# Kernel optimization log

Hardware: AMD Instinct MI355X
Metric: run time of the kernel (lower is better)

The kernel has to match this reference:

```python
import jax, jax.numpy as jnp
import numpy as np

V, E, C, H = 50000, 300, 128, 128
B, SC, SE = 128, 512, 64


def gru_scan(x, lengths, gate_w, gate_b, cand_w, cand_b):
    """TF GRUCell dynamic_rnn: x [B,S,E] -> outputs [B,S,C], zeroed past lengths."""
    Bn, S, _ = x.shape
    Cn = cand_w.shape[1]

    def step(h, inp):
        xt, t = inp  # xt [B,E]
        ru = jax.nn.sigmoid(jnp.concatenate([xt, h], axis=-1) @ gate_w + gate_b)
        r, u = jnp.split(ru, 2, axis=-1)
        c = jnp.tanh(jnp.concatenate([xt, r * h], axis=-1) @ cand_w + cand_b)
        hn = u * h + (1.0 - u) * c
        active = (t < lengths)[:, None]
        hn = jnp.where(active, hn, h)
        out = jnp.where(active, hn, 0.0)
        return hn, out

    h0 = jnp.zeros((Bn, Cn), dtype=x.dtype)
    _, outs = jax.lax.scan(step, h0, (jnp.swapaxes(x, 0, 1), jnp.arange(S)))
    return jnp.swapaxes(outs, 0, 1)


def reverse_seq(x, lengths):
    """tf.reverse_sequence along time for [B,S,D]."""
    S = x.shape[1]
    t = jnp.arange(S)[None, :]
    L = lengths[:, None]
    idx = jnp.where(t < L, L - 1 - t, t)
    return jnp.take_along_axis(x, idx[:, :, None], axis=1)


def attend(states, att_v, att_w, att_b):
    # states [B,S,C]
    scores = jnp.einsum('bsd,d->bs', jnp.tanh(jnp.einsum('bsc,cd->bsd', states, att_w) + att_b), att_v)
    w = jax.nn.softmax(scores, axis=1)
    return jnp.einsum('bsc,bs->bc', states, w)


def extract_features(seq, lengths, embeddings,
                     fw_gate_w, fw_gate_b, fw_cand_w, fw_cand_b,
                     bw_gate_w, bw_gate_b, bw_cand_w, bw_cand_b,
                     att_v, att_w, att_b):
    emb = embeddings[seq]  # [B,S,E]
    fw_states = gru_scan(emb, lengths, fw_gate_w, fw_gate_b, fw_cand_w, fw_cand_b)
    emb_rev = reverse_seq(emb, lengths)
    bw_out = gru_scan(emb_rev, lengths, bw_gate_w, bw_gate_b, bw_cand_w, bw_cand_b)
    bw_states = reverse_seq(bw_out, lengths)
    fw_c = attend(fw_states, att_v, att_w, att_b)
    bw_c = attend(bw_states, att_v, att_w, att_b)
    return jnp.concatenate([fw_c, bw_c], axis=1)


def setup_inputs() -> dict:
    key = jax.random.key(0)
    ks = jax.random.split(key, 20)
    s = 0.05
    context = jax.random.randint(ks[0], (B, SC), 0, V, dtype=jnp.int32)
    end = jax.random.randint(ks[1], (B, SE), 0, V, dtype=jnp.int32)
    context_length = jnp.clip(jax.random.randint(ks[2], (B,), 1, SC + 1), 1, SC).astype(jnp.int32)
    end_length = jnp.clip(jax.random.randint(ks[3], (B,), 1, SE + 1), 1, SE).astype(jnp.int32)
    return {
        'context': context, 'end': end,
        'context_length': context_length, 'end_length': end_length,
        'embeddings': jax.random.normal(ks[4], (V, E), jnp.float32) * s,
        'fw_gate_w': jax.random.normal(ks[5], (E + C, 2 * C), jnp.float32) * s,
        'fw_gate_b': jnp.ones((2 * C,), jnp.float32),
        'fw_cand_w': jax.random.normal(ks[6], (E + C, C), jnp.float32) * s,
        'fw_cand_b': jnp.zeros((C,), jnp.float32),
        'bw_gate_w': jax.random.normal(ks[7], (E + C, 2 * C), jnp.float32) * s,
        'bw_gate_b': jnp.ones((2 * C,), jnp.float32),
        'bw_cand_w': jax.random.normal(ks[8], (E + C, C), jnp.float32) * s,
        'bw_cand_b': jnp.zeros((C,), jnp.float32),
        'att_v': jax.random.normal(ks[9], (C,), jnp.float32) * s,
        'att_w': jax.random.normal(ks[10], (C, C), jnp.float32) * s,
        'att_b': jnp.zeros((C,), jnp.float32),
        'hid_w': jax.random.normal(ks[11], (4 * C, H), jnp.float32) * s,
        'hid_b': jnp.zeros((H,), jnp.float32),
        'out_w': jax.random.normal(ks[12], (H, 1), jnp.float32) * s,
        'out_b': jnp.zeros((1,), jnp.float32),
    }


def reference(context, end, context_length, end_length, embeddings,
              fw_gate_w, fw_gate_b, fw_cand_w, fw_cand_b,
              bw_gate_w, bw_gate_b, bw_cand_w, bw_cand_b,
              att_v, att_w, att_b, hid_w, hid_b, out_w, out_b):
    ctx_f = extract_features(context, context_length, embeddings,
                             fw_gate_w, fw_gate_b, fw_cand_w, fw_cand_b,
                             bw_gate_w, bw_gate_b, bw_cand_w, bw_cand_b,
                             att_v, att_w, att_b)
    end_f = extract_features(end, end_length, embeddings,
                             fw_gate_w, fw_gate_b, fw_cand_w, fw_cand_b,
                             bw_gate_w, bw_gate_b, bw_cand_w, bw_cand_b,
                             att_v, att_w, att_b)
    feats = jnp.concatenate([ctx_f, end_f], axis=1)  # [B, 4C]
    hidden = jax.nn.relu(feats @ hid_w + hid_b)
    logit = (hidden @ out_w + out_b)[:, 0]  # [B]
    return logit
```

## Files before the change

### kernel.cpp

```cpp
#include <hip/hip_runtime.h>
#include <cstdint>
#include <cmath>

static constexpr int V_  = 50000;
static constexpr int E_  = 300;
static constexpr int C_  = 128;
static constexpr int B_  = 128;
static constexpr int SC_ = 512;
static constexpr int SE_ = 64;
static constexpr int NCOL = 768;
static constexpr int KP  = 320;

static constexpr size_t OFF_PROJ  = 0;
static constexpr size_t SZ_PROJ   = (size_t)V_ * NCOL;
static constexpr size_t OFF_WXP   = OFF_PROJ + SZ_PROJ;
static constexpr size_t SZ_WXP    = (size_t)304 * NCOL;
static constexpr size_t OFF_UALL  = OFF_WXP + SZ_WXP;
static constexpr size_t SZ_UALL   = (size_t)C_ * NCOL;
static constexpr size_t OFF_BIAS  = OFF_UALL + SZ_UALL;
static constexpr size_t SZ_BIAS   = NCOL;
static constexpr size_t OFF_ST    = OFF_BIAS + SZ_BIAS;
static constexpr size_t SZ_ST_CTX = (size_t)B_ * SC_ * C_;
static constexpr size_t SZ_ST_END = (size_t)B_ * SE_ * C_;
static constexpr size_t SZ_ST     = 2*SZ_ST_CTX + 2*SZ_ST_END;
static constexpr size_t OFF_FEATS = OFF_ST + SZ_ST;
static constexpr size_t SZ_FEATS  = (size_t)B_ * 512;
static constexpr size_t OFF_BT    = OFF_FEATS + SZ_FEATS;
static constexpr size_t SZ_BT     = (size_t)NCOL * KP / 2 * 2;
static constexpr size_t OFF_AWT   = OFF_BT + SZ_BT;

typedef __attribute__((ext_vector_type(8))) short bf16x8;
typedef __attribute__((ext_vector_type(4))) float f32x4;

static __device__ __forceinline__ unsigned short f2bf_rne(float f) {
  unsigned u = __float_as_uint(f);
  unsigned r = u + 0x7fffu + ((u >> 16) & 1u);
  return (unsigned short)(r >> 16);
}

static __device__ __forceinline__ void gload_lds16(const short* g, short* l) {
  __builtin_amdgcn_global_load_lds(
      (const __attribute__((address_space(1))) void*)g,
      (__attribute__((address_space(3))) void*)l, 16, 0, 0);
}

static __device__ __forceinline__ float fast_sigmoid(float x) {
  return __builtin_amdgcn_rcpf(1.f + __expf(-x));
}
static __device__ __forceinline__ float fast_tanh(float x) {
  return fmaf(-2.f, __builtin_amdgcn_rcpf(__expf(2.f * x) + 1.f), 1.f);
}

__global__ void pack_kernel(const float* __restrict__ fw_gw, const float* __restrict__ fw_gb,
                            const float* __restrict__ fw_cw, const float* __restrict__ fw_cb,
                            const float* __restrict__ bw_gw, const float* __restrict__ bw_gb,
                            const float* __restrict__ bw_cw, const float* __restrict__ bw_cb,
                            float* __restrict__ ws) {
  int i = blockIdx.x * 256 + threadIdx.x;
  float* Wxp  = ws + OFF_WXP;
  float* Uall = ws + OFF_UALL;
  float* bias = ws + OFF_BIAS;
  if (i < 304 * NCOL) {
    int k = i / NCOL, c = i % NCOL;
    float v = 0.f;
    if (k < 300) {
      if (c < 256)      v = fw_gw[k*256 + c];
      else if (c < 384) v = fw_cw[k*128 + (c-256)];
      else if (c < 640) v = bw_gw[k*256 + (c-384)];
      else              v = bw_cw[k*128 + (c-640)];
    }
    Wxp[i] = v;
    return;
  }
  int j = i - 304 * NCOL;
  if (j >= 0 && j < 128 * NCOL) {
    int k = j / NCOL, c = j % NCOL;
    int kk = 300 + k;
    float v;
    if (c < 256)      v = fw_gw[kk*256 + c];
    else if (c < 384) v = fw_cw[kk*128 + (c-256)];
    else if (c < 640) v = bw_gw[kk*256 + (c-384)];
    else              v = bw_cw[kk*128 + (c-640)];
    Uall[j] = v;
    return;
  }
  int m = j - 128 * NCOL;
  if (m >= 0 && m < NCOL) {
    float v;
    if (m < 256)      v = fw_gb[m];
    else if (m < 384) v = fw_cb[m-256];
    else if (m < 640) v = bw_gb[m-384];
    else              v = bw_cb[m-640];
    bias[m] = v;
  }
}

__global__ void pack_bt(const float* __restrict__ Wxp, short* __restrict__ Bthi,
                        short* __restrict__ Btlo, const float* __restrict__ att_w,
                        short* __restrict__ awt_hi, short* __restrict__ awt_lo) {
  int i = blockIdx.x * 256 + threadIdx.x;
  if (i < NCOL * KP) {
    int k = i % KP, n = i / KP;
    float v = (k < 304) ? Wxp[(size_t)k * NCOL + n] : 0.f;
    unsigned short h = f2bf_rne(v);
    float hf = __uint_as_float((unsigned)h << 16);
    unsigned short lo = f2bf_rne(v - hf);
    Bthi[i] = (short)h;
    Btlo[i] = (short)lo;
    return;
  }
  int j = i - NCOL * KP;
  if (j < 128 * 128) {
    int d = j >> 7, c = j & 127;
    float v = att_w[(size_t)c * 128 + d];
    unsigned short h = f2bf_rne(v);
    float hf = __uint_as_float((unsigned)h << 16);
    unsigned short lo = f2bf_rne(v - hf);
    awt_hi[j] = (short)h;
    awt_lo[j] = (short)lo;
  }
}

__global__ void pack_emb(const float* __restrict__ emb, short* __restrict__ Ahi,
                         short* __restrict__ Alo) {
  size_t i = (size_t)blockIdx.x * 256 + threadIdx.x;
  if (i >= (size_t)V_ * KP) return;
  int k = (int)(i % KP);
  size_t row = i / KP;
  float v = (k < E_) ? emb[row * E_ + k] : 0.f;
  unsigned short h = f2bf_rne(v);
  float hf = __uint_as_float((unsigned)h << 16);
  unsigned short lo = f2bf_rne(v - hf);
  Ahi[i] = (short)h;
  Alo[i] = (short)lo;
}

__global__ __launch_bounds__(256) void gemm_mfma(
    const short* __restrict__ Ahi, const short* __restrict__ Alo,
    const short* __restrict__ Bthi, const short* __restrict__ Btlo,
    float* __restrict__ proj) {
  __shared__ short lds[16384];
  int tid = threadIdx.x, wid = tid >> 6, lane = tid & 63;
  int n0 = blockIdx.x * 128, m0 = blockIdx.y * 128;
  f32x4 acc[4][4] = {};

  int lr = lane >> 2, lc = lane & 3;
  int q0 = wid * 2, q1 = q0 + 1;
  int r0 = q0 * 16 + lr, r1 = q1 * 16 + lr;
  int am0 = m0 + r0; if (am0 > V_ - 1) am0 = V_ - 1;
  int am1 = m0 + r1; if (am1 > V_ - 1) am1 = V_ - 1;
  size_t gaOff0 = (size_t)am0 * KP + lc * 8;
  size_t gaOff1 = (size_t)am1 * KP + lc * 8;
  size_t gbOff0 = (size_t)(n0 + r0) * KP + lc * 8;
  size_t gbOff1 = (size_t)(n0 + r1) * KP + lc * 8;

  int quad = lane >> 4;
  int arow = (wid >> 1) * 64 + (lane & 15);
  int brow = (wid & 1) * 64 + (lane & 15);

  for (int k0 = 0; k0 < KP; k0 += 32) {
    gload_lds16(Ahi  + gaOff0 + k0, lds +         q0 * 512);
    gload_lds16(Ahi  + gaOff1 + k0, lds +         q1 * 512);
    gload_lds16(Alo  + gaOff0 + k0, lds +  4096 + q0 * 512);
    gload_lds16(Alo  + gaOff1 + k0, lds +  4096 + q1 * 512);
    gload_lds16(Bthi + gbOff0 + k0, lds +  8192 + q0 * 512);
    gload_lds16(Bthi + gbOff1 + k0, lds +  8192 + q1 * 512);
    gload_lds16(Btlo + gbOff0 + k0, lds + 12288 + q0 * 512);
    gload_lds16(Btlo + gbOff1 + k0, lds + 12288 + q1 * 512);
    __syncthreads();

    bf16x8 ah[4], al[4], bh[4], bl[4];
#pragma unroll
    for (int i = 0; i < 4; ++i) {
      ah[i] = *(bf16x8*)&lds[        (arow + i*16) * 32 + quad * 8];
      al[i] = *(bf16x8*)&lds[ 4096 + (arow + i*16) * 32 + quad * 8];
      bh[i] = *(bf16x8*)&lds[ 8192 + (brow + i*16) * 32 + quad * 8];
      bl[i] = *(bf16x8*)&lds[12288 + (brow + i*16) * 32 + quad * 8];
    }
#pragma unroll
    for (int i = 0; i < 4; ++i)
#pragma unroll
      for (int j = 0; j < 4; ++j) {
        acc[i][j] = __builtin_amdgcn_mfma_f32_16x16x32_bf16(ah[i], bh[j], acc[i][j], 0, 0, 0);
        acc[i][j] = __builtin_amdgcn_mfma_f32_16x16x32_bf16(ah[i], bl[j], acc[i][j], 0, 0, 0);
        acc[i][j] = __builtin_amdgcn_mfma_f32_16x16x32_bf16(al[i], bh[j], acc[i][j], 0, 0, 0);
      }
    __syncthreads();
  }

  int colb = n0 + (wid & 1) * 64 + (lane & 15);
  int rowb = m0 + (wid >> 1) * 64 + quad * 4;
#pragma unroll
  for (int i = 0; i < 4; ++i) {
    int rb = rowb + i * 16;
#pragma unroll
    for (int j = 0; j < 4; ++j) {
      int cc = colb + j * 16;
#pragma unroll
      for (int r = 0; r < 4; ++r) {
        int rr = rb + r;
        if (rr < V_) proj[(size_t)rr * NCOL + cc] = acc[i][j][r];
      }
    }
  }
}

__global__ __attribute__((amdgpu_flat_work_group_size(256, 256),
                          amdgpu_waves_per_eu(2, 2)))
void recur_kernel(
    const int* __restrict__ ctx, const int* __restrict__ endseq,
    const int* __restrict__ ctx_len, const int* __restrict__ end_len,
    const float* __restrict__ proj, const float* __restrict__ Uall,
    const float* __restrict__ bias, float* __restrict__ states) {
  __shared__ __align__(16) float h_s[128];
  __shared__ __align__(16) float rh_s[128];
  __shared__ __align__(16) float u_s[128];
  __shared__ __align__(16) float pg[8][260];
  __shared__ __align__(16) float pc[8][132];

  int bid = blockIdx.x;
  int tid = threadIdx.x;
  const int* seq; int S, L, b, dir; float* stbase;
  if (bid < 256) {
    b = bid >> 1; dir = bid & 1;
    seq = ctx + b * SC_; S = SC_; L = ctx_len[b];
    stbase = states + (dir ? SZ_ST_CTX : 0) + (size_t)b * SC_ * C_;
  } else {
    int q = bid - 256; b = q >> 1; dir = q & 1;
    seq = endseq + b * SE_; S = SE_; L = end_len[b];
    stbase = states + 2*SZ_ST_CTX + (dir ? SZ_ST_END : 0) + (size_t)b * SE_ * C_;
  }
  int dirOff = dir ? 384 : 0;
  int kg = tid >> 5, jg = tid & 31;

  float wg[16][8];
  float wc[16][4];
#pragma unroll
  for (int kk = 0; kk < 16; ++kk) {
    const float* up = Uall + (size_t)(kg*16 + kk) * NCOL + dirOff;
    float4 w0 = *(const float4*)(up + jg*8);
    float4 w1 = *(const float4*)(up + jg*8 + 4);
    wg[kk][0]=w0.x; wg[kk][1]=w0.y; wg[kk][2]=w0.z; wg[kk][3]=w0.w;
    wg[kk][4]=w1.x; wg[kk][5]=w1.y; wg[kk][6]=w1.z; wg[kk][7]=w1.w;
    float4 wv = *(const float4*)(up + 256 + jg*4);
    wc[kk][0]=wv.x; wc[kk][1]=wv.y; wc[kk][2]=wv.z; wc[kk][3]=wv.w;
  }
  float bias_g = bias[dirOff + tid];
  float bias_c = (tid < 128) ? bias[dirOff + 256 + tid] : 0.f;

  if (tid < 128) h_s[tid] = 0.f;
  __syncthreads();

  int pos0 = dir ? (L - 1) : 0;
  int tok0 = seq[pos0];
  const float* xr0 = proj + (size_t)tok0 * NCOL + dirOff;
  float xg = xr0[tid];
  float xc = (tid < 128) ? xr0[256 + tid] : 0.f;

  for (int t = 0; t < L; ++t) {
    float xg_n = 0.f, xc_n = 0.f;
    if (t + 1 < L) {
      int pos_n = dir ? (L - 2 - t) : (t + 1);
      int tok_n = seq[pos_n];
      const float* xr = proj + (size_t)tok_n * NCOL + dirOff;
      xg_n = xr[tid];
      xc_n = (tid < 128) ? xr[256 + tid] : 0.f;
    }

    float a[8] = {0.f,0.f,0.f,0.f,0.f,0.f,0.f,0.f};
    const float4* h4 = (const float4*)h_s;
#pragma unroll
    for (int q = 0; q < 4; ++q) {
      float4 hv = h4[kg*4 + q];
      float he[4] = {hv.x, hv.y, hv.z, hv.w};
#pragma unroll
      for (int e = 0; e < 4; ++e)
#pragma unroll
        for (int jj = 0; jj < 8; ++jj)
          a[jj] += he[e] * wg[q*4 + e][jj];
    }
    *(float4*)(&pg[kg][jg*8])     = make_float4(a[0], a[1], a[2], a[3]);
    *(float4*)(&pg[kg][jg*8 + 4]) = make_float4(a[4], a[5], a[6], a[7]);
    __syncthreads();

    float g = xg + bias_g;
#pragma unroll
    for (int k2 = 0; k2 < 8; ++k2) g += pg[k2][tid];
    g = fast_sigmoid(g);

    float h_old = 0.f;
    if (tid < 128) { h_old = h_s[tid]; rh_s[tid] = g * h_old; }
    else           { u_s[tid - 128] = g; }
    __syncthreads();

    float ac[4] = {0.f, 0.f, 0.f, 0.f};
    const float4* rh4 = (const float4*)rh_s;
#pragma unroll
    for (int q = 0; q < 4; ++q) {
      float4 rv = rh4[kg*4 + q];
      float re[4] = {rv.x, rv.y, rv.z, rv.w};
#pragma unroll
      for (int e = 0; e < 4; ++e)
#pragma unroll
        for (int jj = 0; jj < 4; ++jj)
          ac[jj] += re[e] * wc[q*4 + e][jj];
    }
    *(float4*)(&pc[kg][jg*4]) = make_float4(ac[0], ac[1], ac[2], ac[3]);
    __syncthreads();

    if (tid < 128) {
      float cs = xc + bias_c;
#pragma unroll
      for (int k2 = 0; k2 < 8; ++k2) cs += pc[k2][tid];
      float c = fast_tanh(cs);
      float u = u_s[tid];
      float hn = u * h_old + (1.f - u) * c;
      h_s[tid] = hn;
      int pos = dir ? (L - 1 - t) : t;
      stbase[(size_t)pos * C_ + tid] = hn;
    }
    __syncthreads();
    xg = xg_n; xc = xc_n;
  }

  for (int i = L * C_ + tid; i < S * C_; i += 256) stbase[i] = 0.f;
}

__global__ __launch_bounds__(256, 2) void attn_kernel(
    const float* __restrict__ states, const short* __restrict__ awt_hi,
    const short* __restrict__ awt_lo, const float* __restrict__ att_v,
    const float* __restrict__ att_b, float* __restrict__ feats) {
  __shared__ __align__(16) float st_s[16][132];
  __shared__ __align__(16) short ah_s[16][132];
  __shared__ __align__(16) short al_s[16][132];
  __shared__ float spart[4][16];
  __shared__ float score_s[16];
  __shared__ float cm[128], cl[128], ca[128];

  int bid = blockIdx.x, tid = threadIdx.x;
  int b, dir, S, featOff; const float* stb;
  if (bid < 256) {
    b = bid >> 1; dir = bid & 1; S = SC_;
    stb = states + (dir ? SZ_ST_CTX : 0) + (size_t)b * SC_ * C_;
    featOff = dir * 128;
  } else {
    int q = bid - 256; b = q >> 1; dir = q & 1; S = SE_;
    stb = states + 2*SZ_ST_CTX + (dir ? SZ_ST_END : 0) + (size_t)b * SE_ * C_;
    featOff = 256 + dir * 128;
  }

  int w = tid >> 6, lane = tid & 63;
  int quad = lane >> 4, l15 = lane & 15;

  int d0 = 32 * w + l15, d1 = d0 + 16;
  bf16x8 bh0[4], bh1[4], bl0[4], bl1[4];
#pragma unroll
  for (int kt = 0; kt < 4; ++kt) {
    bh0[kt] = *(const bf16x8*)&awt_hi[d0*128 + kt*32 + quad*8];
    bh1[kt] = *(const bf16x8*)&awt_hi[d1*128 + kt*32 + quad*8];
    bl0[kt] = *(const bf16x8*)&awt_lo[d0*128 + kt*32 + quad*8];
    bl1[kt] = *(const bf16x8*)&awt_lo[d1*128 + kt*32 + quad*8];
  }
  float vv0 = att_v[d0], vv1 = att_v[d1];
  float bb0 = att_b[d0], bb1 = att_b[d1];

  int c = tid & 127, half = tid >> 7;
  float m = -1e30f, lsum = 0.f, acc = 0.f;

  int lrow = tid >> 4, lcol = (tid & 15) * 8;
  float4 p0, p1;
  {
    const float* src = stb + (size_t)lrow * C_ + lcol;
    p0 = *(const float4*)(src);
    p1 = *(const float4*)(src + 4);
  }

  int nchunks = S >> 4;
  for (int ch = 0; ch < nchunks; ++ch) {
    __syncthreads();
    float f[8] = {p0.x, p0.y, p0.z, p0.w, p1.x, p1.y, p1.z, p1.w};
    short hi8[8], lo8[8];
#pragma unroll
    for (int j = 0; j < 8; ++j) {
      unsigned short h = f2bf_rne(f[j]);
      float hf = __uint_as_float((unsigned)h << 16);
      hi8[j] = (short)h;
      lo8[j] = (short)f2bf_rne(f[j] - hf);
    }
    *(float4*)(&st_s[lrow][lcol])     = p0;
    *(float4*)(&st_s[lrow][lcol + 4]) = p1;
    *(bf16x8*)(&ah_s[lrow][lcol]) = *(bf16x8*)hi8;
    *(bf16x8*)(&al_s[lrow][lcol]) = *(bf16x8*)lo8;
    if (ch + 1 < nchunks) {
      const float* src = stb + (size_t)((ch + 1) * 16 + lrow) * C_ + lcol;
      p0 = *(const float4*)(src);
      p1 = *(const float4*)(src + 4);
    }
    __syncthreads();

    f32x4 ac0 = {0.f, 0.f, 0.f, 0.f}, ac1 = {0.f, 0.f, 0.f, 0.f};
#pragma unroll
    for (int kt = 0; kt < 4; ++kt) {
      bf16x8 a_hi = *(bf16x8*)&ah_s[l15][kt*32 + quad*8];
      bf16x8 a_lo = *(bf16x8*)&al_s[l15][kt*32 + quad*8];
      ac0 = __builtin_amdgcn_mfma_f32_16x16x32_bf16(a_hi, bh0[kt], ac0, 0, 0, 0);
      ac0 = __builtin_amdgcn_mfma_f32_16x16x32_bf16(a_hi, bl0[kt], ac0, 0, 0, 0);
      ac0 = __builtin_amdgcn_mfma_f32_16x16x32_bf16(a_lo, bh0[kt], ac0, 0, 0, 0);
      ac1 = __builtin_amdgcn_mfma_f32_16x16x32_bf16(a_hi, bh1[kt], ac1, 0, 0, 0);
      ac1 = __builtin_amdgcn_mfma_f32_16x16x32_bf16(a_hi, bl1[kt], ac1, 0, 0, 0);
      ac1 = __builtin_amdgcn_mfma_f32_16x16x32_bf16(a_lo, bh1[kt], ac1, 0, 0, 0);
    }

    float part[4];
#pragma unroll
    for (int r = 0; r < 4; ++r)
      part[r] = fast_tanh(ac0[r] + bb0) * vv0 + fast_tanh(ac1[r] + bb1) * vv1;
#pragma unroll
    for (int mask = 1; mask <= 8; mask <<= 1)
#pragma unroll
      for (int r = 0; r < 4; ++r)
        part[r] += __shfl_xor(part[r], mask, 64);
    if (l15 == 0) {
#pragma unroll
      for (int r = 0; r < 4; ++r) spart[w][quad*4 + r] = part[r];
    }
    __syncthreads();
    if (tid < 16)
      score_s[tid] = spart[0][tid] + spart[1][tid] + spart[2][tid] + spart[3][tid];
    __syncthreads();

    float srow[8]; float smax = m;
#pragma unroll
    for (int r = 0; r < 8; ++r) { srow[r] = score_s[half*8 + r]; smax = fmaxf(smax, srow[r]); }
    float scale = __expf(m - smax);
    acc *= scale; lsum *= scale; m = smax;
#pragma unroll
    for (int r = 0; r < 8; ++r) {
      float wgt = __expf(srow[r] - m);
      lsum += wgt;
      acc += wgt * st_s[half*8 + r][c];
    }
  }

  __syncthreads();
  if (half == 1) { cm[c] = m; cl[c] = lsum; ca[c] = acc; }
  __syncthreads();
  if (half == 0) {
    float m1 = cm[c], l1 = cl[c], a1 = ca[c];
    float M = fmaxf(m, m1);
    float w0 = __expf(m - M), w1 = __expf(m1 - M);
    feats[b * 512 + featOff + c] = (acc * w0 + a1 * w1) / (lsum * w0 + l1 * w1);
  }
}

__global__ __launch_bounds__(128) void head_kernel(
    const float* __restrict__ feats, const float* __restrict__ hid_w,
    const float* __restrict__ hid_b, const float* __restrict__ out_w,
    const float* __restrict__ out_b, float* __restrict__ out) {
  __shared__ __align__(16) float f_s[512];
  __shared__ float part[2];
  int b = blockIdx.x, tid = threadIdx.x;
  for (int i = tid; i < 512; i += 128) f_s[i] = feats[b * 512 + i];
  __syncthreads();
  float h = hid_b[tid];
  for (int k = 0; k < 512; ++k) h += f_s[k] * hid_w[k * 128 + tid];
  h = fmaxf(h, 0.f);
  float p = h * out_w[tid];
#pragma unroll
  for (int off = 32; off > 0; off >>= 1) p += __shfl_xor(p, off, 64);
  if ((tid & 63) == 0) part[tid >> 6] = p;
  __syncthreads();
  if (tid == 0) out[b] = part[0] + part[1] + out_b[0];
}

extern "C" void kernel_launch(void* const* d_in, const int* in_sizes, int n_in,
                              void* d_out, int out_size, void* d_ws, size_t ws_size,
                              hipStream_t stream) {
  const int*   ctx     = (const int*)d_in[0];
  const int*   endseq  = (const int*)d_in[1];
  const int*   ctx_len = (const int*)d_in[2];
  const int*   end_len = (const int*)d_in[3];
  const float* emb     = (const float*)d_in[4];
  const float* fw_gw   = (const float*)d_in[5];
  const float* fw_gb   = (const float*)d_in[6];
  const float* fw_cw   = (const float*)d_in[7];
  const float* fw_cb   = (const float*)d_in[8];
  const float* bw_gw   = (const float*)d_in[9];
  const float* bw_gb   = (const float*)d_in[10];
  const float* bw_cw   = (const float*)d_in[11];
  const float* bw_cb   = (const float*)d_in[12];
  const float* att_v   = (const float*)d_in[13];
  const float* att_w   = (const float*)d_in[14];
  const float* att_b   = (const float*)d_in[15];
  const float* hid_w   = (const float*)d_in[16];
  const float* hid_b   = (const float*)d_in[17];
  const float* out_w   = (const float*)d_in[18];
  const float* out_b   = (const float*)d_in[19];
  float* ws  = (float*)d_ws;
  float* out = (float*)d_out;

  short* Ahi    = (short*)(ws + OFF_ST);
  short* Alo    = Ahi + (size_t)V_ * KP;
  short* Bthi   = (short*)(ws + OFF_BT);
  short* Btlo   = Bthi + (size_t)NCOL * KP;
  short* awt_hi = (short*)(ws + OFF_AWT);
  short* awt_lo = awt_hi + 128 * 128;

  pack_kernel<<<1299, 256, 0, stream>>>(fw_gw, fw_gb, fw_cw, fw_cb,
                                        bw_gw, bw_gb, bw_cw, bw_cb, ws);
  pack_bt<<<(NCOL * KP + 128 * 128 + 255) / 256, 256, 0, stream>>>(
      ws + OFF_WXP, Bthi, Btlo, att_w, awt_hi, awt_lo);
  pack_emb<<<(int)(((size_t)V_ * KP + 255) / 256), 256, 0, stream>>>(emb, Ahi, Alo);

  dim3 ggrid(6, 391);
  gemm_mfma<<<ggrid, 256, 0, stream>>>(Ahi, Alo, Bthi, Btlo, ws + OFF_PROJ);

  recur_kernel<<<512, 256, 0, stream>>>(ctx, endseq, ctx_len, end_len,
                                        ws + OFF_PROJ, ws + OFF_UALL,
                                        ws + OFF_BIAS, ws + OFF_ST);

  attn_kernel<<<512, 256, 0, stream>>>(ws + OFF_ST, awt_hi, awt_lo,
                                       att_v, att_b, ws + OFF_FEATS);

  head_kernel<<<128, 128, 0, stream>>>(ws + OFF_FEATS, hid_w, hid_b,
                                       out_w, out_b, out);
}
```

Before: 768.4 us.

## Batch GRU recurrence over 16 sequences per block using split-bf16 MFMA

The recurrence kernel no longer runs one sequence per block with scalar FP32 dot products. It now handles 16 sequences per block (32 blocks in total) and computes the gate and candidate matmuls with bf16 MFMA, using a hi/lo split so the result stays close to FP32. This cuts the per-step synchronisations from four to two and replaces the VALU accumulation with matrix cores. The cost is that each block runs until the longest of its 16 sequences ends, and only 32 CUs are occupied. Separately, the projection GEMM switches to a 1D grid with an XCD-aware block remap to improve cache locality.

```diff
diff --git a/kernel.cpp b/kernel.cpp
--- a/kernel.cpp
+++ b/kernel.cpp
@@ -141,7 +141,13 @@
     float* __restrict__ proj) {
   __shared__ short lds[16384];
   int tid = threadIdx.x, wid = tid >> 6, lane = tid & 63;
-  int n0 = blockIdx.x * 128, m0 = blockIdx.y * 128;
+
+  int bid = blockIdx.x;
+  int xcd = bid & 7, idx = bid >> 3;
+  int wgid = (xcd < 2 ? xcd * 294 : 588 + (xcd - 2) * 293) + idx;
+  int m0 = (wgid / 6) * 128;
+  int n0 = (wgid % 6) * 128;
+
   f32x4 acc[4][4] = {};
 
   int lr = lane >> 2, lc = lane & 3;
@@ -206,124 +212,220 @@
 }
 
 __global__ __attribute__((amdgpu_flat_work_group_size(256, 256),
-                          amdgpu_waves_per_eu(2, 2)))
-void recur_kernel(
+                          amdgpu_waves_per_eu(1, 1)))
+void recur_mfma_kernel(
     const int* __restrict__ ctx, const int* __restrict__ endseq,
     const int* __restrict__ ctx_len, const int* __restrict__ end_len,
     const float* __restrict__ proj, const float* __restrict__ Uall,
     const float* __restrict__ bias, float* __restrict__ states) {
-  __shared__ __align__(16) float h_s[128];
-  __shared__ __align__(16) float rh_s[128];
-  __shared__ __align__(16) float u_s[128];
-  __shared__ __align__(16) float pg[8][260];
-  __shared__ __align__(16) float pc[8][132];
-
-  int bid = blockIdx.x;
-  int tid = threadIdx.x;
-  const int* seq; int S, L, b, dir; float* stbase;
-  if (bid < 256) {
-    b = bid >> 1; dir = bid & 1;
-    seq = ctx + b * SC_; S = SC_; L = ctx_len[b];
-    stbase = states + (dir ? SZ_ST_CTX : 0) + (size_t)b * SC_ * C_;
-  } else {
-    int q = bid - 256; b = q >> 1; dir = q & 1;
-    seq = endseq + b * SE_; S = SE_; L = end_len[b];
-    stbase = states + 2*SZ_ST_CTX + (dir ? SZ_ST_END : 0) + (size_t)b * SE_ * C_;
-  }
+  __shared__ __align__(16) short hAh[4][16][32];
+  __shared__ __align__(16) short hAl[4][16][32];
+  __shared__ __align__(16) short rAh[4][16][32];
+  __shared__ __align__(16) short rAl[4][16][32];
+  __shared__ __align__(16) float h_f[16][132];
+  __shared__ __align__(16) float u_f[16][132];
+
+  int g = blockIdx.x, tid = threadIdx.x;
+  int w = tid >> 6, lane = tid & 63, quad = lane >> 4, l15 = lane & 15;
+
+  int isEnd = (g >> 4) & 1, dir = (g >> 3) & 1;
+  int b0 = (g & 7) * 16;
+  int S = isEnd ? SE_ : SC_;
+  const int* seqarr = isEnd ? endseq : ctx;
+  const int* lenarr = isEnd ? end_len : ctx_len;
+  float* stroot = states + (isEnd ? (2*SZ_ST_CTX + (dir ? SZ_ST_END : 0))
+                                  : (dir ? SZ_ST_CTX : 0));
   int dirOff = dir ? 384 : 0;
-  int kg = tid >> 5, jg = tid & 31;
-
-  float wg[16][8];
-  float wc[16][4];
-#pragma unroll
-  for (int kk = 0; kk < 16; ++kk) {
-    const float* up = Uall + (size_t)(kg*16 + kk) * NCOL + dirOff;
-    float4 w0 = *(const float4*)(up + jg*8);
-    float4 w1 = *(const float4*)(up + jg*8 + 4);
-    wg[kk][0]=w0.x; wg[kk][1]=w0.y; wg[kk][2]=w0.z; wg[kk][3]=w0.w;
-    wg[kk][4]=w1.x; wg[kk][5]=w1.y; wg[kk][6]=w1.z; wg[kk][7]=w1.w;
-    float4 wv = *(const float4*)(up + 256 + jg*4);
-    wc[kk][0]=wv.x; wc[kk][1]=wv.y; wc[kk][2]=wv.z; wc[kk][3]=wv.w;
-  }
-  float bias_g = bias[dirOff + tid];
-  float bias_c = (tid < 128) ? bias[dirOff + 256 + tid] : 0.f;
-
-  if (tid < 128) h_s[tid] = 0.f;
+
+  const int* seqp[4]; int Lr[4]; float* stb[4];
+#pragma unroll
+  for (int r = 0; r < 4; ++r) {
+    int b = b0 + quad*4 + r;
+    seqp[r] = seqarr + b * S;
+    Lr[r]   = lenarr[b];
+    stb[r]  = stroot + (size_t)b * S * C_;
+  }
+  int Lm = Lr[0];
+#pragma unroll
+  for (int r = 1; r < 4; ++r) Lm = (Lr[r] > Lm) ? Lr[r] : Lm;
+  { int o = __shfl_xor(Lm, 16, 64); Lm = (o > Lm) ? o : Lm; }
+  { int o = __shfl_xor(Lm, 32, 64); Lm = (o > Lm) ? o : Lm; }
+
+  int colg[4], colc[2];
+#pragma unroll
+  for (int tt = 0; tt < 4; ++tt) colg[tt] = w*64 + tt*16 + l15;
+#pragma unroll
+  for (int tt = 0; tt < 2; ++tt) colc[tt] = w*32 + tt*16 + l15;
+
+  bf16x8 gBh[4][4], gBl[4][4], cBh[2][4], cBl[2][4];
+#pragma unroll
+  for (int tt = 0; tt < 4; ++tt)
+#pragma unroll
+    for (int kt = 0; kt < 4; ++kt) {
+      short h8[8], l8[8];
+#pragma unroll
+      for (int j = 0; j < 8; ++j) {
+        float v = Uall[(size_t)(kt*32 + quad*8 + j) * NCOL + dirOff + colg[tt]];
+        unsigned short hh = f2bf_rne(v);
+        float hf = __uint_as_float((unsigned)hh << 16);
+        h8[j] = (short)hh;
+        l8[j] = (short)f2bf_rne(v - hf);
+      }
+      gBh[tt][kt] = *(bf16x8*)h8;
+      gBl[tt][kt] = *(bf16x8*)l8;
+    }
+#pragma unroll
+  for (int tt = 0; tt < 2; ++tt)
+#pragma unroll
+    for (int kt = 0; kt < 4; ++kt) {
+      short h8[8], l8[8];
+#pragma unroll
+      for (int j = 0; j < 8; ++j) {
+        float v = Uall[(size_t)(kt*32 + quad*8 + j) * NCOL + dirOff + 256 + colc[tt]];
+        unsigned short hh = f2bf_rne(v);
+        float hf = __uint_as_float((unsigned)hh << 16);
+        h8[j] = (short)hh;
+        l8[j] = (short)f2bf_rne(v - hf);
+      }
+      cBh[tt][kt] = *(bf16x8*)h8;
+      cBl[tt][kt] = *(bf16x8*)l8;
+    }
+
+  float bg[4], bc[2];
+#pragma unroll
+  for (int tt = 0; tt < 4; ++tt) bg[tt] = bias[dirOff + colg[tt]];
+#pragma unroll
+  for (int tt = 0; tt < 2; ++tt) bc[tt] = bias[dirOff + 256 + colc[tt]];
+
+  for (int i = tid; i < 16*132; i += 256) ((float*)h_f)[i] = 0.f;
+  for (int i = tid; i < 4*16*32; i += 256) {
+    ((short*)hAh)[i] = 0; ((short*)hAl)[i] = 0;
+  }
   __syncthreads();
 
-  int pos0 = dir ? (L - 1) : 0;
-  int tok0 = seq[pos0];
-  const float* xr0 = proj + (size_t)tok0 * NCOL + dirOff;
-  float xg = xr0[tid];
-  float xc = (tid < 128) ? xr0[256 + tid] : 0.f;
-
-  for (int t = 0; t < L; ++t) {
-    float xg_n = 0.f, xc_n = 0.f;
-    if (t + 1 < L) {
-      int pos_n = dir ? (L - 2 - t) : (t + 1);
-      int tok_n = seq[pos_n];
-      const float* xr = proj + (size_t)tok_n * NCOL + dirOff;
-      xg_n = xr[tid];
-      xc_n = (tid < 128) ? xr[256 + tid] : 0.f;
-    }
-
-    float a[8] = {0.f,0.f,0.f,0.f,0.f,0.f,0.f,0.f};
-    const float4* h4 = (const float4*)h_s;
-#pragma unroll
-    for (int q = 0; q < 4; ++q) {
-      float4 hv = h4[kg*4 + q];
-      float he[4] = {hv.x, hv.y, hv.z, hv.w};
-#pragma unroll
-      for (int e = 0; e < 4; ++e)
-#pragma unroll
-        for (int jj = 0; jj < 8; ++jj)
-          a[jj] += he[e] * wg[q*4 + e][jj];
-    }
-    *(float4*)(&pg[kg][jg*8])     = make_float4(a[0], a[1], a[2], a[3]);
-    *(float4*)(&pg[kg][jg*8 + 4]) = make_float4(a[4], a[5], a[6], a[7]);
-    __syncthreads();
-
-    float g = xg + bias_g;
-#pragma unroll
-    for (int k2 = 0; k2 < 8; ++k2) g += pg[k2][tid];
-    g = fast_sigmoid(g);
-
-    float h_old = 0.f;
-    if (tid < 128) { h_old = h_s[tid]; rh_s[tid] = g * h_old; }
-    else           { u_s[tid - 128] = g; }
-    __syncthreads();
-
-    float ac[4] = {0.f, 0.f, 0.f, 0.f};
-    const float4* rh4 = (const float4*)rh_s;
-#pragma unroll
-    for (int q = 0; q < 4; ++q) {
-      float4 rv = rh4[kg*4 + q];
-      float re[4] = {rv.x, rv.y, rv.z, rv.w};
-#pragma unroll
-      for (int e = 0; e < 4; ++e)
-#pragma unroll
-        for (int jj = 0; jj < 4; ++jj)
-          ac[jj] += re[e] * wc[q*4 + e][jj];
-    }
-    *(float4*)(&pc[kg][jg*4]) = make_float4(ac[0], ac[1], ac[2], ac[3]);
-    __syncthreads();
-
-    if (tid < 128) {
-      float cs = xc + bias_c;
-#pragma unroll
-      for (int k2 = 0; k2 < 8; ++k2) cs += pc[k2][tid];
-      float c = fast_tanh(cs);
-      float u = u_s[tid];
-      float hn = u * h_old + (1.f - u) * c;
-      h_s[tid] = hn;
-      int pos = dir ? (L - 1 - t) : t;
-      stbase[(size_t)pos * C_ + tid] = hn;
-    }
-    __syncthreads();
-    xg = xg_n; xc = xc_n;
-  }
-
-  for (int i = L * C_ + tid; i < S * C_; i += 256) stbase[i] = 0.f;
+  auto load_x = [&](int stp, float (&XG)[4][4], float (&XC)[2][4]) {
+#pragma unroll
+    for (int r = 0; r < 4; ++r) {
+      int L = Lr[r];
+      int pos = (stp < L) ? (dir ? (L - 1 - stp) : stp) : 0;
+      int tok = seqp[r][pos];
+      const float* xr = proj + (size_t)tok * NCOL + dirOff;
+#pragma unroll
+      for (int tt = 0; tt < 4; ++tt) XG[tt][r] = xr[colg[tt]];
+#pragma unroll
+      for (int tt = 0; tt < 2; ++tt) XC[tt][r] = xr[256 + colc[tt]];
+    }
+  };
+
+  float xg[4][4], xc[2][4], xgn[4][4], xcn[2][4];
+  load_x(0, xg, xc);
+
+  for (int t = 0; t < Lm; ++t) {
+    load_x(t + 1, xgn, xcn);
+
+    f32x4 ag[4] = {};
+#pragma unroll
+    for (int kt = 0; kt < 4; ++kt) {
+      bf16x8 Ah = *(bf16x8*)&hAh[kt][l15][quad*8];
+      bf16x8 Al = *(bf16x8*)&hAl[kt][l15][quad*8];
+#pragma unroll
+      for (int tt = 0; tt < 4; ++tt)
+        ag[tt] = __builtin_amdgcn_mfma_f32_16x16x32_bf16(Ah, gBh[tt][kt], ag[tt], 0, 0, 0);
+#pragma unroll
+      for (int tt = 0; tt < 4; ++tt)
+        ag[tt] = __builtin_amdgcn_mfma_f32_16x16x32_bf16(Ah, gBl[tt][kt], ag[tt], 0, 0, 0);
+#pragma unroll
+      for (int tt = 0; tt < 4; ++tt)
+        ag[tt] = __builtin_amdgcn_mfma_f32_16x16x32_bf16(Al, gBh[tt][kt], ag[tt], 0, 0, 0);
+    }
+
+    if (w < 2) {
+#pragma unroll
+      for (int tt = 0; tt < 4; ++tt) {
+        int col = colg[tt];
+        int kt2 = col >> 5, kk = col & 31;
+#pragma unroll
+        for (int r = 0; r < 4; ++r) {
+          int row = quad*4 + r;
+          float gg = fast_sigmoid(ag[tt][r] + xg[tt][r] + bg[tt]);
+          float rh = gg * h_f[row][col];
+          unsigned short hi = f2bf_rne(rh);
+          float hf = __uint_as_float((unsigned)hi << 16);
+          rAh[kt2][row][kk] = (short)hi;
+          rAl[kt2][row][kk] = (short)f2bf_rne(rh - hf);
+        }
+      }
+    } else {
+#pragma unroll
+      for (int tt = 0; tt < 4; ++tt) {
+        int col = colg[tt] - 128;
+#pragma unroll
+        for (int r = 0; r < 4; ++r) {
+          int row = quad*4 + r;
+          float gg = fast_sigmoid(ag[tt][r] + xg[tt][r] + bg[tt]);
+          u_f[row][col] = gg;
+        }
+      }
+    }
+    __syncthreads();
+
+    f32x4 ac[2] = {};
+#pragma unroll
+    for (int kt = 0; kt < 4; ++kt) {
+      bf16x8 Ah = *(bf16x8*)&rAh[kt][l15][quad*8];
+      bf16x8 Al = *(bf16x8*)&rAl[kt][l15][quad*8];
+#pragma unroll
+      for (int tt = 0; tt < 2; ++tt)
+        ac[tt] = __builtin_amdgcn_mfma_f32_16x16x32_bf16(Ah, cBh[tt][kt], ac[tt], 0, 0, 0);
+#pragma unroll
+      for (int tt = 0; tt < 2; ++tt)
+        ac[tt] = __builtin_amdgcn_mfma_f32_16x16x32_bf16(Ah, cBl[tt][kt], ac[tt], 0, 0, 0);
+#pragma unroll
+      for (int tt = 0; tt < 2; ++tt)
+        ac[tt] = __builtin_amdgcn_mfma_f32_16x16x32_bf16(Al, cBh[tt][kt], ac[tt], 0, 0, 0);
+    }
+
+#pragma unroll
+    for (int tt = 0; tt < 2; ++tt) {
+      int col = colc[tt];
+      int kt2 = col >> 5, kk = col & 31;
+#pragma unroll
+      for (int r = 0; r < 4; ++r) {
+        int row = quad*4 + r;
+        float cs = ac[tt][r] + xc[tt][r] + bc[tt];
+        float cd = fast_tanh(cs);
+        float uu = u_f[row][col];
+        float ho = h_f[row][col];
+        float hn = uu * ho + (1.f - uu) * cd;
+        if (t < Lr[r]) {
+          h_f[row][col] = hn;
+          unsigned short hi = f2bf_rne(hn);
+          float hf = __uint_as_float((unsigned)hi << 16);
+          hAh[kt2][row][kk] = (short)hi;
+          hAl[kt2][row][kk] = (short)f2bf_rne(hn - hf);
+          int pos = dir ? (Lr[r] - 1 - t) : t;
+          stb[r][(size_t)pos * C_ + col] = hn;
+        }
+      }
+    }
+    __syncthreads();
+
+#pragma unroll
+    for (int tt = 0; tt < 4; ++tt)
+#pragma unroll
+      for (int r = 0; r < 4; ++r) xg[tt][r] = xgn[tt][r];
+#pragma unroll
+    for (int tt = 0; tt < 2; ++tt)
+#pragma unroll
+      for (int r = 0; r < 4; ++r) xc[tt][r] = xcn[tt][r];
+  }
+
+  for (int i = 0; i < 16; ++i) {
+    int b = b0 + i;
+    int L = lenarr[b];
+    float* sb = stroot + (size_t)b * S * C_;
+    for (int idx = L * C_ + tid; idx < S * C_; idx += 256) sb[idx] = 0.f;
+  }
 }
 
 __global__ __launch_bounds__(256, 2) void attn_kernel(
@@ -512,12 +614,11 @@
       ws + OFF_WXP, Bthi, Btlo, att_w, awt_hi, awt_lo);
   pack_emb<<<(int)(((size_t)V_ * KP + 255) / 256), 256, 0, stream>>>(emb, Ahi, Alo);
 
-  dim3 ggrid(6, 391);
-  gemm_mfma<<<ggrid, 256, 0, stream>>>(Ahi, Alo, Bthi, Btlo, ws + OFF_PROJ);
-
-  recur_kernel<<<512, 256, 0, stream>>>(ctx, endseq, ctx_len, end_len,
-                                        ws + OFF_PROJ, ws + OFF_UALL,
-                                        ws + OFF_BIAS, ws + OFF_ST);
+  gemm_mfma<<<2346, 256, 0, stream>>>(Ahi, Alo, Bthi, Btlo, ws + OFF_PROJ);
+
+  recur_mfma_kernel<<<32, 256, 0, stream>>>(ctx, endseq, ctx_len, end_len,
+                                            ws + OFF_PROJ, ws + OFF_UALL,
+                                            ws + OFF_BIAS, ws + OFF_ST);
 
   attn_kernel<<<512, 256, 0, stream>>>(ws + OFF_ST, awt_hi, awt_lo,
                                        att_v, att_b, ws + OFF_FEATS);
```

Measured after the change: 2.082 ms. 2.71x slower.

## Double recurrence block to 512 threads and remap GEMM tiles per XCD

Applied to the files above, without the earlier changes.

The GRU recurrence kernel now runs 512 threads per block. Each thread holds half as many recurrent-weight rows in registers, so the per-step serial matvec is shorter, and the 16 partial sums are combined with a tree reduction in LDS. Separately, the GEMM grid is flattened to 1D and block ids are remapped so each XCD gets a contiguous range of M-tiles, which should improve L2 reuse of the A rows shared across N-tiles. The cost is more threads per barrier and a longer reduction per step, and 512-thread blocks may lower residency in the recurrence.

```diff
diff --git a/kernel.cpp b/kernel.cpp
--- a/kernel.cpp
+++ b/kernel.cpp
@@ -141,7 +141,13 @@
     float* __restrict__ proj) {
   __shared__ short lds[16384];
   int tid = threadIdx.x, wid = tid >> 6, lane = tid & 63;
-  int n0 = blockIdx.x * 128, m0 = blockIdx.y * 128;
+
+  int bid = blockIdx.x;
+  int xcd = bid & 7, idx = bid >> 3;
+  int wgid = (xcd < 2 ? xcd * 294 : 588 + (xcd - 2) * 293) + idx;
+  int m0 = (wgid / 6) * 128;
+  int n0 = (wgid % 6) * 128;
+
   f32x4 acc[4][4] = {};
 
   int lr = lane >> 2, lc = lane & 3;
@@ -205,7 +211,7 @@
   }
 }
 
-__global__ __attribute__((amdgpu_flat_work_group_size(256, 256),
+__global__ __attribute__((amdgpu_flat_work_group_size(512, 512),
                           amdgpu_waves_per_eu(2, 2)))
 void recur_kernel(
     const int* __restrict__ ctx, const int* __restrict__ endseq,
@@ -215,8 +221,8 @@
   __shared__ __align__(16) float h_s[128];
   __shared__ __align__(16) float rh_s[128];
   __shared__ __align__(16) float u_s[128];
-  __shared__ __align__(16) float pg[8][260];
-  __shared__ __align__(16) float pc[8][132];
+  __shared__ __align__(16) float pg[16][260];
+  __shared__ __align__(16) float pc[16][132];
 
   int bid = blockIdx.x;
   int tid = threadIdx.x;
@@ -233,11 +239,11 @@
   int dirOff = dir ? 384 : 0;
   int kg = tid >> 5, jg = tid & 31;
 
-  float wg[16][8];
-  float wc[16][4];
-#pragma unroll
-  for (int kk = 0; kk < 16; ++kk) {
-    const float* up = Uall + (size_t)(kg*16 + kk) * NCOL + dirOff;
+  float wg[8][8];
+  float wc[8][4];
+#pragma unroll
+  for (int kk = 0; kk < 8; ++kk) {
+    const float* up = Uall + (size_t)(kg*8 + kk) * NCOL + dirOff;
     float4 w0 = *(const float4*)(up + jg*8);
     float4 w1 = *(const float4*)(up + jg*8 + 4);
     wg[kk][0]=w0.x; wg[kk][1]=w0.y; wg[kk][2]=w0.z; wg[kk][3]=w0.w;
@@ -245,7 +251,7 @@
     float4 wv = *(const float4*)(up + 256 + jg*4);
     wc[kk][0]=wv.x; wc[kk][1]=wv.y; wc[kk][2]=wv.z; wc[kk][3]=wv.w;
   }
-  float bias_g = bias[dirOff + tid];
+  float bias_g = (tid < 256) ? bias[dirOff + tid] : 0.f;
   float bias_c = (tid < 128) ? bias[dirOff + 256 + tid] : 0.f;
 
   if (tid < 128) h_s[tid] = 0.f;
@@ -254,7 +260,7 @@
   int pos0 = dir ? (L - 1) : 0;
   int tok0 = seq[pos0];
   const float* xr0 = proj + (size_t)tok0 * NCOL + dirOff;
-  float xg = xr0[tid];
+  float xg = (tid < 256) ? xr0[tid] : 0.f;
   float xc = (tid < 128) ? xr0[256 + tid] : 0.f;
 
   for (int t = 0; t < L; ++t) {
@@ -263,15 +269,15 @@
       int pos_n = dir ? (L - 2 - t) : (t + 1);
       int tok_n = seq[pos_n];
       const float* xr = proj + (size_t)tok_n * NCOL + dirOff;
-      xg_n = xr[tid];
-      xc_n = (tid < 128) ? xr[256 + tid] : 0.f;
+      if (tid < 256) xg_n = xr[tid];
+      if (tid < 128) xc_n = xr[256 + tid];
     }
 
     float a[8] = {0.f,0.f,0.f,0.f,0.f,0.f,0.f,0.f};
     const float4* h4 = (const float4*)h_s;
 #pragma unroll
-    for (int q = 0; q < 4; ++q) {
-      float4 hv = h4[kg*4 + q];
+    for (int q = 0; q < 2; ++q) {
+      float4 hv = h4[kg*2 + q];
       float he[4] = {hv.x, hv.y, hv.z, hv.w};
 #pragma unroll
       for (int e = 0; e < 4; ++e)
@@ -283,21 +289,26 @@
     *(float4*)(&pg[kg][jg*8 + 4]) = make_float4(a[4], a[5], a[6], a[7]);
     __syncthreads();
 
-    float g = xg + bias_g;
-#pragma unroll
-    for (int k2 = 0; k2 < 8; ++k2) g += pg[k2][tid];
-    g = fast_sigmoid(g);
-
     float h_old = 0.f;
-    if (tid < 128) { h_old = h_s[tid]; rh_s[tid] = g * h_old; }
-    else           { u_s[tid - 128] = g; }
+    if (tid < 256) {
+      float s[16];
+#pragma unroll
+      for (int k2 = 0; k2 < 16; ++k2) s[k2] = pg[k2][tid];
+#pragma unroll
+      for (int st = 1; st < 16; st <<= 1)
+#pragma unroll
+        for (int k2 = 0; k2 < 16; k2 += 2*st) s[k2] += s[k2 + st];
+      float g = fast_sigmoid(s[0] + xg + bias_g);
+      if (tid < 128) { h_old = h_s[tid]; rh_s[tid] = g * h_old; }
+      else           { u_s[tid - 128] = g; }
+    }
     __syncthreads();
 
     float ac[4] = {0.f, 0.f, 0.f, 0.f};
     const float4* rh4 = (const float4*)rh_s;
 #pragma unroll
-    for (int q = 0; q < 4; ++q) {
-      float4 rv = rh4[kg*4 + q];
+    for (int q = 0; q < 2; ++q) {
+      float4 rv = rh4[kg*2 + q];
       float re[4] = {rv.x, rv.y, rv.z, rv.w};
 #pragma unroll
       for (int e = 0; e < 4; ++e)
@@ -309,10 +320,14 @@
     __syncthreads();
 
     if (tid < 128) {
-      float cs = xc + bias_c;
-#pragma unroll
-      for (int k2 = 0; k2 < 8; ++k2) cs += pc[k2][tid];
-      float c = fast_tanh(cs);
+      float s[16];
+#pragma unroll
+      for (int k2 = 0; k2 < 16; ++k2) s[k2] = pc[k2][tid];
+#pragma unroll
+      for (int st = 1; st < 16; st <<= 1)
+#pragma unroll
+        for (int k2 = 0; k2 < 16; k2 += 2*st) s[k2] += s[k2 + st];
+      float c = fast_tanh(s[0] + xc + bias_c);
       float u = u_s[tid];
       float hn = u * h_old + (1.f - u) * c;
       h_s[tid] = hn;
@@ -323,7 +338,7 @@
     xg = xg_n; xc = xc_n;
   }
 
-  for (int i = L * C_ + tid; i < S * C_; i += 256) stbase[i] = 0.f;
+  for (int i = L * C_ + tid; i < S * C_; i += 512) stbase[i] = 0.f;
 }
 
 __global__ __launch_bounds__(256, 2) void attn_kernel(
@@ -512,10 +527,9 @@
       ws + OFF_WXP, Bthi, Btlo, att_w, awt_hi, awt_lo);
   pack_emb<<<(int)(((size_t)V_ * KP + 255) / 256), 256, 0, stream>>>(emb, Ahi, Alo);
 
-  dim3 ggrid(6, 391);
-  gemm_mfma<<<ggrid, 256, 0, stream>>>(Ahi, Alo, Bthi, Btlo, ws + OFF_PROJ);
-
-  recur_kernel<<<512, 256, 0, stream>>>(ctx, endseq, ctx_len, end_len,
+  gemm_mfma<<<2346, 256, 0, stream>>>(Ahi, Alo, Bthi, Btlo, ws + OFF_PROJ);
+
+  recur_kernel<<<512, 512, 0, stream>>>(ctx, endseq, ctx_len, end_len,
                                         ws + OFF_PROJ, ws + OFF_UALL,
                                         ws + OFF_BIAS, ws + OFF_ST);
 
```

Measured after the change: 770.3 us. No clear change (+0.2%).

## Split context attention into two halves with merge kernel; remap GEMM grid per XCD

Applied to the files above, without the earlier changes.

The attention kernel now splits each 512-step context chain across two workgroups, each covering 16 chunks. Partial softmax statistics go to a scratch buffer, and a new merge kernel combines them, so the attention stage gets more parallelism. End-sequence chains write a neutral second partial so the merge stays uniform. The GEMM is launched on a 1D grid with an XCD-aware remapping of block IDs to tiles, intended to improve L2 locality. Occupancy hint for attention is raised to 3, at the cost of an extra launch and partial-buffer traffic that reuses the Bt workspace region.

```diff
diff --git a/kernel.cpp b/kernel.cpp
--- a/kernel.cpp
+++ b/kernel.cpp
@@ -141,7 +141,13 @@
     float* __restrict__ proj) {
   __shared__ short lds[16384];
   int tid = threadIdx.x, wid = tid >> 6, lane = tid & 63;
-  int n0 = blockIdx.x * 128, m0 = blockIdx.y * 128;
+
+  int bid = blockIdx.x;
+  int xcd = bid & 7, idx = bid >> 3;
+  int wgid = (xcd < 2 ? xcd * 294 : 588 + (xcd - 2) * 293) + idx;
+  int m0 = (wgid / 6) * 128;
+  int n0 = (wgid % 6) * 128;
+
   f32x4 acc[4][4] = {};
 
   int lr = lane >> 2, lc = lane & 3;
@@ -326,10 +332,10 @@
   for (int i = L * C_ + tid; i < S * C_; i += 256) stbase[i] = 0.f;
 }
 
-__global__ __launch_bounds__(256, 2) void attn_kernel(
+__global__ __launch_bounds__(256, 3) void attn_kernel(
     const float* __restrict__ states, const short* __restrict__ awt_hi,
     const short* __restrict__ awt_lo, const float* __restrict__ att_v,
-    const float* __restrict__ att_b, float* __restrict__ feats) {
+    const float* __restrict__ att_b, float* __restrict__ partials) {
   __shared__ __align__(16) float st_s[16][132];
   __shared__ __align__(16) short ah_s[16][132];
   __shared__ __align__(16) short al_s[16][132];
@@ -338,16 +344,19 @@
   __shared__ float cm[128], cl[128], ca[128];
 
   int bid = blockIdx.x, tid = threadIdx.x;
-  int b, dir, S, featOff; const float* stb;
-  if (bid < 256) {
-    b = bid >> 1; dir = bid & 1; S = SC_;
+  int b, dir, S, pchain, ph, ch0, ch1, isEndWG; const float* stb;
+  if (bid < 512) {
+    int chain = bid >> 1;  ph = bid & 1;
+    b = chain >> 1; dir = chain & 1; S = SC_;
     stb = states + (dir ? SZ_ST_CTX : 0) + (size_t)b * SC_ * C_;
-    featOff = dir * 128;
+    pchain = chain; ch0 = ph * 16; ch1 = ch0 + 16; isEndWG = 0;
   } else {
-    int q = bid - 256; b = q >> 1; dir = q & 1; S = SE_;
+    int e = bid - 512;
+    b = e >> 1; dir = e & 1; S = SE_;
     stb = states + 2*SZ_ST_CTX + (dir ? SZ_ST_END : 0) + (size_t)b * SE_ * C_;
-    featOff = 256 + dir * 128;
-  }
+    pchain = 256 + e; ph = 0; ch0 = 0; ch1 = SE_ >> 4; isEndWG = 1;
+  }
+  (void)S;
 
   int w = tid >> 6, lane = tid & 63;
   int quad = lane >> 4, l15 = lane & 15;
@@ -370,13 +379,12 @@
   int lrow = tid >> 4, lcol = (tid & 15) * 8;
   float4 p0, p1;
   {
-    const float* src = stb + (size_t)lrow * C_ + lcol;
+    const float* src = stb + (size_t)(ch0 * 16 + lrow) * C_ + lcol;
     p0 = *(const float4*)(src);
     p1 = *(const float4*)(src + 4);
   }
 
-  int nchunks = S >> 4;
-  for (int ch = 0; ch < nchunks; ++ch) {
+  for (int ch = ch0; ch < ch1; ++ch) {
     __syncthreads();
     float f[8] = {p0.x, p0.y, p0.z, p0.w, p1.x, p1.y, p1.z, p1.w};
     short hi8[8], lo8[8];
@@ -391,7 +399,7 @@
     *(float4*)(&st_s[lrow][lcol + 4]) = p1;
     *(bf16x8*)(&ah_s[lrow][lcol]) = *(bf16x8*)hi8;
     *(bf16x8*)(&al_s[lrow][lcol]) = *(bf16x8*)lo8;
-    if (ch + 1 < nchunks) {
+    if (ch + 1 < ch1) {
       const float* src = stb + (size_t)((ch + 1) * 16 + lrow) * C_ + lcol;
       p0 = *(const float4*)(src);
       p1 = *(const float4*)(src + 4);
@@ -449,8 +457,32 @@
     float m1 = cm[c], l1 = cl[c], a1 = ca[c];
     float M = fmaxf(m, m1);
     float w0 = __expf(m - M), w1 = __expf(m1 - M);
-    feats[b * 512 + featOff + c] = (acc * w0 + a1 * w1) / (lsum * w0 + l1 * w1);
-  }
+    float Lt = lsum * w0 + l1 * w1;
+    float At = acc * w0 + a1 * w1;
+    float* p = partials + ((size_t)pchain * 2 + ph) * 130;
+    if (c == 0) { p[0] = M; p[1] = Lt; }
+    p[2 + c] = At;
+    if (isEndWG) {
+      float* pn = partials + ((size_t)pchain * 2 + 1) * 130;
+      if (c == 0) { pn[0] = -1e30f; pn[1] = 0.f; }
+      pn[2 + c] = 0.f;
+    }
+  }
+}
+
+__global__ __launch_bounds__(128) void attn_merge_kernel(
+    const float* __restrict__ partials, float* __restrict__ feats) {
+  int q = blockIdx.x, c = threadIdx.x;
+  const float* p0 = partials + (size_t)q * 2 * 130;
+  const float* p1 = p0 + 130;
+  float m0 = p0[0], l0 = p0[1], a0 = p0[2 + c];
+  float m1 = p1[0], l1 = p1[1], a1 = p1[2 + c];
+  float M = fmaxf(m0, m1);
+  float w0 = __expf(m0 - M), w1 = __expf(m1 - M);
+  int b, off;
+  if (q < 256) { b = q >> 1; off = (q & 1) * 128; }
+  else { int e = q - 256; b = e >> 1; off = 256 + (e & 1) * 128; }
+  feats[b * 512 + off + c] = (a0 * w0 + a1 * w1) / (l0 * w0 + l1 * w1);
 }
 
 __global__ __launch_bounds__(128) void head_kernel(
@@ -505,6 +537,7 @@
   short* Btlo   = Bthi + (size_t)NCOL * KP;
   short* awt_hi = (short*)(ws + OFF_AWT);
   short* awt_lo = awt_hi + 128 * 128;
+  float* partials = ws + OFF_BT;
 
   pack_kernel<<<1299, 256, 0, stream>>>(fw_gw, fw_gb, fw_cw, fw_cb,
                                         bw_gw, bw_gb, bw_cw, bw_cb, ws);
@@ -512,15 +545,15 @@
       ws + OFF_WXP, Bthi, Btlo, att_w, awt_hi, awt_lo);
   pack_emb<<<(int)(((size_t)V_ * KP + 255) / 256), 256, 0, stream>>>(emb, Ahi, Alo);
 
-  dim3 ggrid(6, 391);
-  gemm_mfma<<<ggrid, 256, 0, stream>>>(Ahi, Alo, Bthi, Btlo, ws + OFF_PROJ);
+  gemm_mfma<<<2346, 256, 0, stream>>>(Ahi, Alo, Bthi, Btlo, ws + OFF_PROJ);
 
   recur_kernel<<<512, 256, 0, stream>>>(ctx, endseq, ctx_len, end_len,
                                         ws + OFF_PROJ, ws + OFF_UALL,
                                         ws + OFF_BIAS, ws + OFF_ST);
 
-  attn_kernel<<<512, 256, 0, stream>>>(ws + OFF_ST, awt_hi, awt_lo,
-                                       att_v, att_b, ws + OFF_FEATS);
+  attn_kernel<<<768, 256, 0, stream>>>(ws + OFF_ST, awt_hi, awt_lo,
+                                       att_v, att_b, partials);
+  attn_merge_kernel<<<512, 128, 0, stream>>>(partials, ws + OFF_FEATS);
 
   head_kernel<<<128, 128, 0, stream>>>(ws + OFF_FEATS, hid_w, hid_b,
                                        out_w, out_b, out);
```

Result: faster. 739.9 us (-3.7%).
